# Kernel tuning notes

Measured on AMD Instinct MI355X. Metric: run time of the kernel, lower is better.

Reference implementation:

```python
import jax, jax.numpy as jnp
import numpy as np

B, N, E = 64, 20000, 160000
F_TEXT, HID, OUT = 300, 1024, 1664
NEG_SLOPE = 0.2


def setup_inputs() -> dict:
    key = jax.random.key(0)
    ks = jax.random.split(key, 9)
    img_feat = jax.random.normal(ks[0], (B, OUT), dtype=jnp.float32)
    node_features = jax.random.normal(ks[1], (N, F_TEXT), dtype=jnp.float32)
    edge_src = jax.random.randint(ks[2], (E,), 0, N, dtype=jnp.int32)
    edge_dst = jax.random.randint(ks[3], (E,), 0, N, dtype=jnp.int32)
    edge_weight = jax.random.uniform(ks[4], (E,), dtype=jnp.float32)
    W1 = jax.random.normal(ks[5], (F_TEXT, HID), dtype=jnp.float32) / np.sqrt(F_TEXT)
    b1 = jax.random.normal(ks[6], (HID,), dtype=jnp.float32) * 0.01
    W2 = jax.random.normal(ks[7], (HID, OUT), dtype=jnp.float32) / np.sqrt(HID)
    b2 = jax.random.normal(ks[8], (OUT,), dtype=jnp.float32) * 0.01
    return {"img_feat": img_feat, "node_features": node_features,
            "edge_src": edge_src, "edge_dst": edge_dst, "edge_weight": edge_weight,
            "W1": W1, "b1": b1, "W2": W2, "b2": b2}


def _gcn_norm(edge_src, edge_dst, edge_weight, num_nodes):
    # PyG gcn_norm with add_self_loops=False: symmetric degree normalization
    deg = jax.ops.segment_sum(edge_weight, edge_dst, num_segments=num_nodes)
    dinv = jnp.where(deg > 0, jax.lax.rsqrt(deg), 0.0)
    return dinv[edge_src] * edge_weight * dinv[edge_dst]


def _gcn_conv(x, edge_src, edge_dst, norm, W, b):
    # GCNConv: linear transform, then normalized gather -> scatter-add, then bias
    h = x @ W  # [N, out]
    msgs = h[edge_src] * norm[:, None]  # [E, out] gather + scale
    agg = jax.ops.segment_sum(msgs, edge_dst, num_segments=x.shape[0])
    return agg + b


def reference(img_feat, node_features, edge_src, edge_dst, edge_weight, W1, b1, W2, b2):
    num_nodes = node_features.shape[0]
    norm = _gcn_norm(edge_src, edge_dst, edge_weight, num_nodes)
    x = _gcn_conv(node_features, edge_src, edge_dst, norm, W1, b1)
    x = jnp.where(x >= 0, x, NEG_SLOPE * x)  # leaky_relu(0.2)
    x = _gcn_conv(x, edge_src, edge_dst, norm, W2, b2)
    return img_feat @ x.T  # [B, N]
```

## Files before the change

kernel.cpp:

```cpp
#include <hip/hip_runtime.h>
#include <hip/hip_bf16.h>

#define NNODES 20000
#define NEDGES 160000
#define BQ     64
#define FTEXT  300
#define KPAD1  320
#define HIDDIM 1024
#define OUTDIM 1664
#define EB     (NEDGES / 256)
#define SPLITK 13
#define KLEN   (OUTDIM / SPLITK)

typedef __attribute__((ext_vector_type(8))) short short8;
typedef __attribute__((ext_vector_type(4))) float floatx4;

__device__ inline unsigned short f2bf(float f) {
    union { float f; unsigned int u; } v; v.f = f;
    unsigned int r = v.u + 0x7FFF + ((v.u >> 16) & 1);
    return (unsigned short)(r >> 16);
}
__device__ inline float bf2f(unsigned short h) {
    union { unsigned int u; float f; } v; v.u = ((unsigned int)h) << 16;
    return v.f;
}

__device__ inline void gload16(const unsigned short* g, unsigned short* l) {
    __builtin_amdgcn_global_load_lds(
        (const __attribute__((address_space(1))) unsigned int*)g,
        (__attribute__((address_space(3))) unsigned int*)l, 16, 0, 0);
}

#define W1N  (HIDDIM * KPAD1)
#define N1F4 (HIDDIM * OUTDIM / 4)
#define N2F4 (BQ * OUTDIM / 4)
#define N3F4 (NNODES * FTEXT / 4)
__global__ __launch_bounds__(256) void prep_kernel(
        const int* __restrict__ dst, const float* __restrict__ w,
        float* __restrict__ deg, int* __restrict__ cnt,
        const float* __restrict__ W1, unsigned short* __restrict__ W1ch,
        const float* __restrict__ W2, unsigned short* __restrict__ W2b,
        const float* __restrict__ img, unsigned short* __restrict__ imgb,
        const float* __restrict__ nf, unsigned short* __restrict__ nfb) {
    if (blockIdx.x < EB) {
        int e = blockIdx.x * 256 + threadIdx.x;
        int d = dst[e];
        atomicAdd(&deg[d], w[e]);
        atomicAdd(&cnt[d], 1);
        return;
    }
    int i = (blockIdx.x - EB) * 256 + threadIdx.x;
    if (i < W1N) {
        int p   = i / 20480;
        int ww  = i - p * 20480;
        int s   = ww >> 11;
        int lq  = (ww >> 9) & 3;
        int col = (ww >> 3) & 63;
        int j   = ww & 7;
        int n = p * 64 + col;
        int k = s * 32 + lq * 8 + j;
        float v = (k < FTEXT) ? W1[(long)k * HIDDIM + n] : 0.f;
        W1ch[i] = f2bf(v);
        return;
    }
    i -= W1N;
    const float* in; unsigned short* outp; int j;
    if (i < N1F4)                    { in = W2;  outp = W2b;  j = i; }
    else if (i < N1F4 + N2F4)        { in = img; outp = imgb; j = i - N1F4; }
    else if (i < N1F4 + N2F4 + N3F4) { in = nf;  outp = nfb;  j = i - N1F4 - N2F4; }
    else return;
    float4 v = ((const float4*)in)[j];
    ushort4 o;
    o.x = f2bf(v.x); o.y = f2bf(v.y); o.z = f2bf(v.z); o.w = f2bf(v.w);
    ((ushort4*)outp)[j] = o;
}

__global__ __launch_bounds__(1024) void scan_kernel(const int* __restrict__ cnt,
                                                    int* __restrict__ row_start, int N) {
    __shared__ int partial[1024];
    const int CH = 20;
    int t = threadIdx.x;
    int begin = t * CH;
    int nloc = N - begin; if (nloc > CH) nloc = CH; if (nloc < 0) nloc = 0;
    int vals[CH];
    int s = 0;
    if (nloc == CH) {
        #pragma unroll
        for (int i = 0; i < CH / 4; i++) {
            int4 v = ((const int4*)(cnt + begin))[i];
            vals[i*4+0] = v.x; vals[i*4+1] = v.y; vals[i*4+2] = v.z; vals[i*4+3] = v.w;
            s += v.x + v.y + v.z + v.w;
        }
    } else {
        for (int i = 0; i < nloc; i++) { vals[i] = cnt[begin + i]; s += vals[i]; }
    }
    partial[t] = s;
    __syncthreads();
    for (int off = 1; off < 1024; off <<= 1) {
        int v = (t >= off) ? partial[t - off] : 0;
        __syncthreads();
        partial[t] += v;
        __syncthreads();
    }
    int run = (t == 0) ? 0 : partial[t - 1];
    for (int i = 0; i < nloc; i++) { row_start[begin + i] = run; run += vals[i]; }
    if (t == 1023) row_start[N] = partial[1023];
}

__global__ __launch_bounds__(256) void fillgemm_kernel(
        const int* __restrict__ dst, const int* __restrict__ src,
        const float* __restrict__ w, const float* __restrict__ deg,
        const int* __restrict__ row_start, int* __restrict__ cursor,
        int* __restrict__ src_s, float* __restrict__ wnrm_s,
        const unsigned short* __restrict__ imgb, const unsigned short* __restrict__ W2b,
        float* __restrict__ Ztf13) {
    __shared__ unsigned short As[128][40];
    __shared__ unsigned short Bs[64][40];
    if (blockIdx.x < EB) {
        int e = blockIdx.x * 256 + threadIdx.x;
        int d = dst[e], s = src[e];
        float dd = deg[d], ds = deg[s];
        float nv = (ds > 0.f ? rsqrtf(ds) : 0.f) * w[e] * (dd > 0.f ? rsqrtf(dd) : 0.f);
        int pos = row_start[d] + atomicAdd(&cursor[d], 1);
        src_s[pos] = s;
        wnrm_s[pos] = nv;
        return;
    }
    int bb = blockIdx.x - EB;
    int n0 = (bb & 15) * 64;
    int z  = bb >> 4;
    int kbeg = z * KLEN;
    int t = threadIdx.x;
    int wave = t >> 6, lane = t & 63;
    int lm = lane & 15, lq = lane >> 4;
    floatx4 acc[2][4] = {};
    for (int k0 = kbeg; k0 < kbeg + KLEN; k0 += 32) {
        #pragma unroll
        for (int p2 = 0; p2 < 2; p2++) {
            int idx = p2 * 256 + t;
            int r = idx >> 2, c8 = (idx & 3) * 8;
            uint4 v = make_uint4(0, 0, 0, 0);
            if (r < BQ) v = *(const uint4*)(imgb + (long)r * OUTDIM + k0 + c8);
            *(uint4*)&As[r][c8] = v;
        }
        {
            int r = t >> 2, c8 = (t & 3) * 8;
            uint4 v = *(const uint4*)(W2b + (long)(n0 + r) * OUTDIM + k0 + c8);
            *(uint4*)&Bs[r][c8] = v;
        }
        __syncthreads();
        short8 a[2], b[4];
        #pragma unroll
        for (int rt = 0; rt < 2; rt++)
            a[rt] = *(const short8*)&As[wave * 32 + rt * 16 + lm][lq * 8];
        #pragma unroll
        for (int ct = 0; ct < 4; ct++)
            b[ct] = *(const short8*)&Bs[ct * 16 + lm][lq * 8];
        #pragma unroll
        for (int rt = 0; rt < 2; rt++)
            #pragma unroll
            for (int ct = 0; ct < 4; ct++)
                acc[rt][ct] = __builtin_amdgcn_mfma_f32_16x16x32_bf16(
                    a[rt], b[ct], acc[rt][ct], 0, 0, 0);
        __syncthreads();
    }
    #pragma unroll
    for (int rt = 0; rt < 2; rt++)
        #pragma unroll
        for (int r = 0; r < 4; r++) {
            int gm = wave * 32 + rt * 16 + lq * 4 + r;
            if (gm >= BQ) continue;
            #pragma unroll
            for (int ct = 0; ct < 4; ct++)
                Ztf13[(long)z * BQ * HIDDIM + (long)gm * HIDDIM + n0 + ct * 16 + lm]
                    = acc[rt][ct][r];
        }
}

__global__ __launch_bounds__(256) void aggzt_kernel(
        const unsigned short* __restrict__ nfb, const int* __restrict__ row_start,
        const int* __restrict__ src_s, const float* __restrict__ wnrm_s,
        unsigned short* __restrict__ out,
        const float* __restrict__ Ztf13, unsigned short* __restrict__ Zt,
        const float* __restrict__ img, const float* __restrict__ b2,
        float* __restrict__ cvec) {
    __shared__ float red[256];
    if (blockIdx.x < NNODES / 4) {
        int wave = threadIdx.x >> 6, lane = threadIdx.x & 63;
        int d = blockIdx.x * 4 + wave;
        int s0 = row_start[d], s1 = row_start[d + 1];
        float4 acc  = make_float4(0.f, 0.f, 0.f, 0.f);
        float4 acc2 = make_float4(0.f, 0.f, 0.f, 0.f);
        for (int base = s0; base < s1; base += 64) {
            int m = s1 - base; if (m > 64) m = 64;
            int   src_l = (lane < m) ? src_s[base + lane]  : 0;
            float w_l   = (lane < m) ? wnrm_s[base + lane] : 0.f;
            int sj = __shfl(src_l, 0);
            float wj = __shfl(w_l, 0);
            const ushort4* row = (const ushort4*)(nfb + (long)sj * FTEXT);
            ushort4 hv  = row[lane];
            ushort4 hv2 = make_ushort4(0, 0, 0, 0);
            if (lane < 11) hv2 = row[64 + lane];
            for (int j = 0; j < m; j++) {
                ushort4 nv  = make_ushort4(0, 0, 0, 0);
                ushort4 nv2 = make_ushort4(0, 0, 0, 0);
                float wn = 0.f;
                if (j + 1 < m) {
                    int sn = __shfl(src_l, j + 1);
                    wn = __shfl(w_l, j + 1);
                    const ushort4* nrow = (const ushort4*)(nfb + (long)sn * FTEXT);
                    nv = nrow[lane];
                    if (lane < 11) nv2 = nrow[64 + lane];
                }
                acc.x  += bf2f(hv.x)  * wj; acc.y  += bf2f(hv.y)  * wj;
                acc.z  += bf2f(hv.z)  * wj; acc.w  += bf2f(hv.w)  * wj;
                acc2.x += bf2f(hv2.x) * wj; acc2.y += bf2f(hv2.y) * wj;
                acc2.z += bf2f(hv2.z) * wj; acc2.w += bf2f(hv2.w) * wj;
                hv = nv; hv2 = nv2; wj = wn;
            }
        }
        unsigned short* orow = out + (long)d * KPAD1;
        ushort4 o;
        o.x = f2bf(acc.x); o.y = f2bf(acc.y); o.z = f2bf(acc.z); o.w = f2bf(acc.w);
        ((ushort4*)orow)[lane] = o;
        if (lane < 16) {
            ushort4 o2 = make_ushort4(0, 0, 0, 0);
            if (lane < 11) {
                o2.x = f2bf(acc2.x); o2.y = f2bf(acc2.y);
                o2.z = f2bf(acc2.z); o2.w = f2bf(acc2.w);
            }
            ((ushort4*)orow)[64 + lane] = o2;
        }
        return;
    }
    int bb = blockIdx.x - NNODES / 4;
    if (bb < (BQ * HIDDIM) / 256) {
        int i = bb * 256 + threadIdx.x;
        float s = 0.f;
        #pragma unroll
        for (int z = 0; z < SPLITK; z++) s += Ztf13[(long)z * BQ * HIDDIM + i];
        Zt[i] = f2bf(s);
    } else {
        int b = bb - (BQ * HIDDIM) / 256;
        int l = threadIdx.x;
        float v = 0.f;
        for (int f = l; f < OUTDIM; f += 256) v += img[(long)b * OUTDIM + f] * b2[f];
        red[l] = v;
        __syncthreads();
        if (l < 64) {
            v = red[l] + red[l + 64] + red[l + 128] + red[l + 192];
            for (int off = 32; off > 0; off >>= 1) v += __shfl_down(v, off);
            if (l == 0) cvec[b] = v;
        }
    }
}

__global__ __launch_bounds__(256, 3) void xy_gemm(
        const unsigned short* __restrict__ aggNF, const unsigned short* __restrict__ W1ch,
        const float* __restrict__ b1, const unsigned short* __restrict__ Zt,
        float* __restrict__ Y, int M) {
    __shared__ unsigned short Bsh[20480];
    __shared__ unsigned short xs[32][76];
    int t = threadIdx.x;
    int wn = t >> 6, lane = t & 63;
    int lm = lane & 15, lq = lane >> 4;
    int m0 = blockIdx.x * 32;

    short8 afr[2][10];
    #pragma unroll
    for (int rt = 0; rt < 2; rt++) {
        const unsigned short* ap = aggNF + (long)(m0 + rt * 16 + lm) * KPAD1 + lq * 8;
        #pragma unroll
        for (int kk = 0; kk < 10; kk++)
            afr[rt][kk] = *(const short8*)(ap + kk * 32);
    }
    {
        const unsigned short* src = W1ch + t * 8;
        #pragma unroll
        for (int r = 0; r < 10; r++)
            gload16(src + r * 2048, &Bsh[t * 8 + r * 2048]);
    }
    floatx4 yacc[2] = {};
    for (int p = 0; p < 16; p++) {
        __syncthreads();
        floatx4 acc[2] = {};
        #pragma unroll
        for (int s = 0; s < 10; s++) {
            short8 b = *(const short8*)&Bsh[s * 2048 + lq * 512 + (wn * 16 + lm) * 8];
            acc[0] = __builtin_amdgcn_mfma_f32_16x16x32_bf16(afr[0][s], b, acc[0], 0, 0, 0);
            acc[1] = __builtin_amdgcn_mfma_f32_16x16x32_bf16(afr[1][s], b, acc[1], 0, 0, 0);
        }
        {
            int col = wn * 16 + lm;
            float bv = b1[p * 64 + col];
            #pragma unroll
            for (int rt = 0; rt < 2; rt++)
                #pragma unroll
                for (int r = 0; r < 4; r++) {
                    float v = acc[rt][r] + bv;
                    v = v >= 0.f ? v : 0.2f * v;
                    xs[rt * 16 + lq * 4 + r][col] = f2bf(v);
                }
        }
        __syncthreads();
        if (p + 1 < 16) {
            const unsigned short* src = W1ch + (long)(p + 1) * 20480 + t * 8;
            #pragma unroll
            for (int r = 0; r < 10; r++)
                gload16(src + r * 2048, &Bsh[t * 8 + r * 2048]);
        }
        #pragma unroll
        for (int kk = 0; kk < 2; kk++) {
            short8 b = *(const short8*)(Zt + (long)(wn * 16 + lm) * HIDDIM
                                            + p * 64 + kk * 32 + lq * 8);
            #pragma unroll
            for (int rt = 0; rt < 2; rt++) {
                short8 a = *(const short8*)&xs[rt * 16 + lm][kk * 32 + lq * 8];
                yacc[rt] = __builtin_amdgcn_mfma_f32_16x16x32_bf16(a, b, yacc[rt], 0, 0, 0);
            }
        }
    }
    #pragma unroll
    for (int rt = 0; rt < 2; rt++)
        #pragma unroll
        for (int r = 0; r < 4; r++)
            Y[(long)(m0 + rt * 16 + lq * 4 + r) * 64 + wn * 16 + lm] = yacc[rt][r];
}

__global__ __launch_bounds__(256) void outagg_kernel(const float* __restrict__ Y,
        const int* __restrict__ row_start, const int* __restrict__ src_s,
        const float* __restrict__ wnrm_s, const float* __restrict__ c,
        float* __restrict__ out, int N) {
    __shared__ float tile[4][68];
    int d0 = blockIdx.x * 4;
    int t = threadIdx.x;
    int wave = t >> 6, lane = t & 63;
    int d = d0 + wave;
    int s0 = row_start[d], s1 = row_start[d + 1];
    float acc = 0.f;
    for (int base = s0; base < s1; base += 64) {
        int m = s1 - base; if (m > 64) m = 64;
        int   src_l = (lane < m) ? src_s[base + lane]  : 0;
        float w_l   = (lane < m) ? wnrm_s[base + lane] : 0.f;
        int sj = __shfl(src_l, 0);
        float wj = __shfl(w_l, 0);
        float yv = Y[(long)sj * 64 + lane];
        for (int j = 0; j < m; j++) {
            float yn = 0.f, wn = 0.f;
            if (j + 1 < m) {
                int sn = __shfl(src_l, j + 1);
                wn = __shfl(w_l, j + 1);
                yn = Y[(long)sn * 64 + lane];
            }
            acc += wj * yv;
            yv = yn; wj = wn;
        }
    }
    tile[wave][lane] = acc + c[lane];
    __syncthreads();
    int b = t >> 2, j = t & 3;
    out[(long)b * N + d0 + j] = tile[j][b];
}

extern "C" void kernel_launch(void* const* d_in, const int* in_sizes, int n_in,
                              void* d_out, int out_size, void* d_ws, size_t ws_size,
                              hipStream_t stream) {
    const float* img_feat      = (const float*)d_in[0];
    const float* node_features = (const float*)d_in[1];
    const int*   edge_src      = (const int*)d_in[2];
    const int*   edge_dst      = (const int*)d_in[3];
    const float* edge_weight   = (const float*)d_in[4];
    const float* W1            = (const float*)d_in[5];
    const float* b1            = (const float*)d_in[6];
    const float* W2            = (const float*)d_in[7];
    const float* b2            = (const float*)d_in[8];
    float* out = (float*)d_out;

    const int N = NNODES;

    char* ws = (char*)d_ws;
    size_t off = 0;
    auto alloc = [&](size_t bytes) -> void* {
        void* p = ws + off;
        off = (off + bytes + 255) & ~(size_t)255;
        return p;
    };
    float*          deg       = (float*)alloc((size_t)N * 4);
    int*            cnt       = (int*)alloc((size_t)N * 4);
    int*            cursor    = (int*)alloc((size_t)N * 4);
    size_t zero_bytes = off;
    float*          Ztf13     = (float*)alloc((size_t)SPLITK * BQ * HIDDIM * 4);
    float*          Y         = (float*)alloc((size_t)N * BQ * 4);
    int*            row_start = (int*)alloc((size_t)(N + 1) * 4);
    int*            src_s     = (int*)alloc((size_t)NEDGES * 4);
    float*          wnrm_s    = (float*)alloc((size_t)NEDGES * 4);
    unsigned short* aggNF     = (unsigned short*)alloc((size_t)N * KPAD1 * 2);
    unsigned short* W1ch      = (unsigned short*)alloc((size_t)HIDDIM * KPAD1 * 2);
    unsigned short* W2b       = (unsigned short*)alloc((size_t)HIDDIM * OUTDIM * 2);
    unsigned short* imgb      = (unsigned short*)alloc((size_t)BQ * OUTDIM * 2);
    unsigned short* nfb       = (unsigned short*)alloc((size_t)N * FTEXT * 2);
    unsigned short* Zt        = (unsigned short*)alloc((size_t)BQ * HIDDIM * 2);
    float*          cvec      = (float*)alloc((size_t)BQ * 4);

    hipMemsetAsync(ws, 0, zero_bytes, stream);

    int cvb = (W1N + N1F4 + N2F4 + N3F4 + 255) / 256;
    prep_kernel<<<EB + cvb, 256, 0, stream>>>(
        edge_dst, edge_weight, deg, cnt,
        W1, W1ch, W2, W2b, img_feat, imgb, node_features, nfb);

    scan_kernel<<<1, 1024, 0, stream>>>(cnt, row_start, N);

    fillgemm_kernel<<<EB + 16 * SPLITK, 256, 0, stream>>>(
        edge_dst, edge_src, edge_weight, deg, row_start, cursor, src_s, wnrm_s,
        imgb, W2b, Ztf13);

    aggzt_kernel<<<NNODES / 4 + (BQ * HIDDIM) / 256 + BQ, 256, 0, stream>>>(
        nfb, row_start, src_s, wnrm_s, aggNF, Ztf13, Zt, img_feat, b2, cvec);

    xy_gemm<<<NNODES / 32, 256, 0, stream>>>(aggNF, W1ch, b1, Zt, Y, N);

    outagg_kernel<<<N / 4, 256, 0, stream>>>(Y, row_start, src_s, wnrm_s, cvec, out, N);
}
```

Before: 215.6 us.

## Regroup kernels: run scan alongside split-K GEMM, move bias dot and Zt reduce earlier

The single-block prefix scan now runs as one block of a combined kernel that also launches the split-K img×W2 GEMM, so the serial scan overlaps with GEMM work instead of running alone. The scan shrinks to 256 threads that read the counts twice instead of caching them. The img·b2 bias dot moves into the prep kernel. The Zt split-K reduction moves into the CSR fill kernel, which leaves aggregation as its own kernel. The launch count stays the same, but the scan per thread is longer and serial.

```diff
diff --git a/kernel.cpp b/kernel.cpp
--- a/kernel.cpp
+++ b/kernel.cpp
@@ -41,7 +41,9 @@
         const float* __restrict__ W1, unsigned short* __restrict__ W1ch,
         const float* __restrict__ W2, unsigned short* __restrict__ W2b,
         const float* __restrict__ img, unsigned short* __restrict__ imgb,
-        const float* __restrict__ nf, unsigned short* __restrict__ nfb) {
+        const float* __restrict__ nf, unsigned short* __restrict__ nfb,
+        const float* __restrict__ b2, float* __restrict__ cvec) {
+    __shared__ float red[256];
     if (blockIdx.x < EB) {
         int e = blockIdx.x * 256 + threadIdx.x;
         int d = dst[e];
@@ -49,7 +51,21 @@
         atomicAdd(&cnt[d], 1);
         return;
     }
-    int i = (blockIdx.x - EB) * 256 + threadIdx.x;
+    if (blockIdx.x < EB + BQ) {
+        int b = blockIdx.x - EB;
+        int l = threadIdx.x;
+        float v = 0.f;
+        for (int f = l; f < OUTDIM; f += 256) v += img[(long)b * OUTDIM + f] * b2[f];
+        red[l] = v;
+        __syncthreads();
+        if (l < 64) {
+            v = red[l] + red[l + 64] + red[l + 128] + red[l + 192];
+            for (int off = 32; off > 0; off >>= 1) v += __shfl_down(v, off);
+            if (l == 0) cvec[b] = v;
+        }
+        return;
+    }
+    int i = (blockIdx.x - EB - BQ) * 256 + threadIdx.x;
     if (i < W1N) {
         int p   = i / 20480;
         int ww  = i - p * 20480;
@@ -75,47 +91,94 @@
     ((ushort4*)outp)[j] = o;
 }
 
-__global__ __launch_bounds__(1024) void scan_kernel(const int* __restrict__ cnt,
-                                                    int* __restrict__ row_start, int N) {
-    __shared__ int partial[1024];
-    const int CH = 20;
+__global__ __launch_bounds__(256) void scangemm_kernel(
+        const int* __restrict__ cnt, int* __restrict__ row_start,
+        const unsigned short* __restrict__ imgb, const unsigned short* __restrict__ W2b,
+        float* __restrict__ Ztf13) {
+    __shared__ unsigned short As[128][40];
+    __shared__ unsigned short Bs[64][40];
+    __shared__ int partial[256];
+    if (blockIdx.x == 0) {
+        const int CH2 = 79;
+        int t = threadIdx.x;
+        int begin = t * CH2;
+        int nloc = NNODES - begin; if (nloc > CH2) nloc = CH2; if (nloc < 0) nloc = 0;
+        int s = 0;
+        for (int i = 0; i < nloc; i++) s += cnt[begin + i];
+        partial[t] = s;
+        __syncthreads();
+        for (int off = 1; off < 256; off <<= 1) {
+            int v = (t >= off) ? partial[t - off] : 0;
+            __syncthreads();
+            partial[t] += v;
+            __syncthreads();
+        }
+        int run = (t == 0) ? 0 : partial[t - 1];
+        for (int i = 0; i < nloc; i++) {
+            int c = cnt[begin + i];
+            row_start[begin + i] = run;
+            run += c;
+        }
+        if (t == 255) row_start[NNODES] = partial[255];
+        return;
+    }
+    int bb = blockIdx.x - 1;
+    int n0 = (bb & 15) * 64;
+    int z  = bb >> 4;
+    int kbeg = z * KLEN;
     int t = threadIdx.x;
-    int begin = t * CH;
-    int nloc = N - begin; if (nloc > CH) nloc = CH; if (nloc < 0) nloc = 0;
-    int vals[CH];
-    int s = 0;
-    if (nloc == CH) {
-        #pragma unroll
-        for (int i = 0; i < CH / 4; i++) {
-            int4 v = ((const int4*)(cnt + begin))[i];
-            vals[i*4+0] = v.x; vals[i*4+1] = v.y; vals[i*4+2] = v.z; vals[i*4+3] = v.w;
-            s += v.x + v.y + v.z + v.w;
-        }
-    } else {
-        for (int i = 0; i < nloc; i++) { vals[i] = cnt[begin + i]; s += vals[i]; }
-    }
-    partial[t] = s;
-    __syncthreads();
-    for (int off = 1; off < 1024; off <<= 1) {
-        int v = (t >= off) ? partial[t - off] : 0;
-        __syncthreads();
-        partial[t] += v;
-        __syncthreads();
-    }
-    int run = (t == 0) ? 0 : partial[t - 1];
-    for (int i = 0; i < nloc; i++) { row_start[begin + i] = run; run += vals[i]; }
-    if (t == 1023) row_start[N] = partial[1023];
-}
-
-__global__ __launch_bounds__(256) void fillgemm_kernel(
+    int wave = t >> 6, lane = t & 63;
+    int lm = lane & 15, lq = lane >> 4;
+    floatx4 acc[2][4] = {};
+    for (int k0 = kbeg; k0 < kbeg + KLEN; k0 += 32) {
+        #pragma unroll
+        for (int p2 = 0; p2 < 2; p2++) {
+            int idx = p2 * 256 + t;
+            int r = idx >> 2, c8 = (idx & 3) * 8;
+            uint4 v = make_uint4(0, 0, 0, 0);
+            if (r < BQ) v = *(const uint4*)(imgb + (long)r * OUTDIM + k0 + c8);
+            *(uint4*)&As[r][c8] = v;
+        }
+        {
+            int r = t >> 2, c8 = (t & 3) * 8;
+            uint4 v = *(const uint4*)(W2b + (long)(n0 + r) * OUTDIM + k0 + c8);
+            *(uint4*)&Bs[r][c8] = v;
+        }
+        __syncthreads();
+        short8 a[2], b[4];
+        #pragma unroll
+        for (int rt = 0; rt < 2; rt++)
+            a[rt] = *(const short8*)&As[wave * 32 + rt * 16 + lm][lq * 8];
+        #pragma unroll
+        for (int ct = 0; ct < 4; ct++)
+            b[ct] = *(const short8*)&Bs[ct * 16 + lm][lq * 8];
+        #pragma unroll
+        for (int rt = 0; rt < 2; rt++)
+            #pragma unroll
+            for (int ct = 0; ct < 4; ct++)
+                acc[rt][ct] = __builtin_amdgcn_mfma_f32_16x16x32_bf16(
+                    a[rt], b[ct], acc[rt][ct], 0, 0, 0);
+        __syncthreads();
+    }
+    #pragma unroll
+    for (int rt = 0; rt < 2; rt++)
+        #pragma unroll
+        for (int r = 0; r < 4; r++) {
+            int gm = wave * 32 + rt * 16 + lq * 4 + r;
+            if (gm >= BQ) continue;
+            #pragma unroll
+            for (int ct = 0; ct < 4; ct++)
+                Ztf13[(long)z * BQ * HIDDIM + (long)gm * HIDDIM + n0 + ct * 16 + lm]
+                    = acc[rt][ct][r];
+        }
+}
+
+__global__ __launch_bounds__(256) void fillzt_kernel(
         const int* __restrict__ dst, const int* __restrict__ src,
         const float* __restrict__ w, const float* __restrict__ deg,
         const int* __restrict__ row_start, int* __restrict__ cursor,
         int* __restrict__ src_s, float* __restrict__ wnrm_s,
-        const unsigned short* __restrict__ imgb, const unsigned short* __restrict__ W2b,
-        float* __restrict__ Ztf13) {
-    __shared__ unsigned short As[128][40];
-    __shared__ unsigned short Bs[64][40];
+        const float* __restrict__ Ztf13, unsigned short* __restrict__ Zt) {
     if (blockIdx.x < EB) {
         int e = blockIdx.x * 256 + threadIdx.x;
         int d = dst[e], s = src[e];
@@ -126,132 +189,61 @@
         wnrm_s[pos] = nv;
         return;
     }
-    int bb = blockIdx.x - EB;
-    int n0 = (bb & 15) * 64;
-    int z  = bb >> 4;
-    int kbeg = z * KLEN;
-    int t = threadIdx.x;
-    int wave = t >> 6, lane = t & 63;
-    int lm = lane & 15, lq = lane >> 4;
-    floatx4 acc[2][4] = {};
-    for (int k0 = kbeg; k0 < kbeg + KLEN; k0 += 32) {
-        #pragma unroll
-        for (int p2 = 0; p2 < 2; p2++) {
-            int idx = p2 * 256 + t;
-            int r = idx >> 2, c8 = (idx & 3) * 8;
-            uint4 v = make_uint4(0, 0, 0, 0);
-            if (r < BQ) v = *(const uint4*)(imgb + (long)r * OUTDIM + k0 + c8);
-            *(uint4*)&As[r][c8] = v;
-        }
-        {
-            int r = t >> 2, c8 = (t & 3) * 8;
-            uint4 v = *(const uint4*)(W2b + (long)(n0 + r) * OUTDIM + k0 + c8);
-            *(uint4*)&Bs[r][c8] = v;
-        }
-        __syncthreads();
-        short8 a[2], b[4];
-        #pragma unroll
-        for (int rt = 0; rt < 2; rt++)
-            a[rt] = *(const short8*)&As[wave * 32 + rt * 16 + lm][lq * 8];
-        #pragma unroll
-        for (int ct = 0; ct < 4; ct++)
-            b[ct] = *(const short8*)&Bs[ct * 16 + lm][lq * 8];
-        #pragma unroll
-        for (int rt = 0; rt < 2; rt++)
-            #pragma unroll
-            for (int ct = 0; ct < 4; ct++)
-                acc[rt][ct] = __builtin_amdgcn_mfma_f32_16x16x32_bf16(
-                    a[rt], b[ct], acc[rt][ct], 0, 0, 0);
-        __syncthreads();
-    }
+    int i = (blockIdx.x - EB) * 256 + threadIdx.x;
+    float s = 0.f;
     #pragma unroll
-    for (int rt = 0; rt < 2; rt++)
-        #pragma unroll
-        for (int r = 0; r < 4; r++) {
-            int gm = wave * 32 + rt * 16 + lq * 4 + r;
-            if (gm >= BQ) continue;
-            #pragma unroll
-            for (int ct = 0; ct < 4; ct++)
-                Ztf13[(long)z * BQ * HIDDIM + (long)gm * HIDDIM + n0 + ct * 16 + lm]
-                    = acc[rt][ct][r];
-        }
-}
-
-__global__ __launch_bounds__(256) void aggzt_kernel(
+    for (int z = 0; z < SPLITK; z++) s += Ztf13[(long)z * BQ * HIDDIM + i];
+    Zt[i] = f2bf(s);
+}
+
+__global__ __launch_bounds__(256) void aggnf_kernel(
         const unsigned short* __restrict__ nfb, const int* __restrict__ row_start,
         const int* __restrict__ src_s, const float* __restrict__ wnrm_s,
-        unsigned short* __restrict__ out,
-        const float* __restrict__ Ztf13, unsigned short* __restrict__ Zt,
-        const float* __restrict__ img, const float* __restrict__ b2,
-        float* __restrict__ cvec) {
-    __shared__ float red[256];
-    if (blockIdx.x < NNODES / 4) {
-        int wave = threadIdx.x >> 6, lane = threadIdx.x & 63;
-        int d = blockIdx.x * 4 + wave;
-        int s0 = row_start[d], s1 = row_start[d + 1];
-        float4 acc  = make_float4(0.f, 0.f, 0.f, 0.f);
-        float4 acc2 = make_float4(0.f, 0.f, 0.f, 0.f);
-        for (int base = s0; base < s1; base += 64) {
-            int m = s1 - base; if (m > 64) m = 64;
-            int   src_l = (lane < m) ? src_s[base + lane]  : 0;
-            float w_l   = (lane < m) ? wnrm_s[base + lane] : 0.f;
-            int sj = __shfl(src_l, 0);
-            float wj = __shfl(w_l, 0);
-            const ushort4* row = (const ushort4*)(nfb + (long)sj * FTEXT);
-            ushort4 hv  = row[lane];
-            ushort4 hv2 = make_ushort4(0, 0, 0, 0);
-            if (lane < 11) hv2 = row[64 + lane];
-            for (int j = 0; j < m; j++) {
-                ushort4 nv  = make_ushort4(0, 0, 0, 0);
-                ushort4 nv2 = make_ushort4(0, 0, 0, 0);
-                float wn = 0.f;
-                if (j + 1 < m) {
-                    int sn = __shfl(src_l, j + 1);
-                    wn = __shfl(w_l, j + 1);
-                    const ushort4* nrow = (const ushort4*)(nfb + (long)sn * FTEXT);
-                    nv = nrow[lane];
-                    if (lane < 11) nv2 = nrow[64 + lane];
-                }
-                acc.x  += bf2f(hv.x)  * wj; acc.y  += bf2f(hv.y)  * wj;
-                acc.z  += bf2f(hv.z)  * wj; acc.w  += bf2f(hv.w)  * wj;
-                acc2.x += bf2f(hv2.x) * wj; acc2.y += bf2f(hv2.y) * wj;
-                acc2.z += bf2f(hv2.z) * wj; acc2.w += bf2f(hv2.w) * wj;
-                hv = nv; hv2 = nv2; wj = wn;
+        unsigned short* __restrict__ out) {
+    int wave = threadIdx.x >> 6, lane = threadIdx.x & 63;
+    int d = blockIdx.x * 4 + wave;
+    int s0 = row_start[d], s1 = row_start[d + 1];
+    float4 acc  = make_float4(0.f, 0.f, 0.f, 0.f);
+    float4 acc2 = make_float4(0.f, 0.f, 0.f, 0.f);
+    for (int base = s0; base < s1; base += 64) {
+        int m = s1 - base; if (m > 64) m = 64;
+        int   src_l = (lane < m) ? src_s[base + lane]  : 0;
+        float w_l   = (lane < m) ? wnrm_s[base + lane] : 0.f;
+        int sj = __shfl(src_l, 0);
+        float wj = __shfl(w_l, 0);
+        const ushort4* row = (const ushort4*)(nfb + (long)sj * FTEXT);
+        ushort4 hv  = row[lane];
+        ushort4 hv2 = make_ushort4(0, 0, 0, 0);
+        if (lane < 11) hv2 = row[64 + lane];
+        for (int j = 0; j < m; j++) {
+            ushort4 nv  = make_ushort4(0, 0, 0, 0);
+            ushort4 nv2 = make_ushort4(0, 0, 0, 0);
+            float wn = 0.f;
+            if (j + 1 < m) {
+                int sn = __shfl(src_l, j + 1);
+                wn = __shfl(w_l, j + 1);
+                const ushort4* nrow = (const ushort4*)(nfb + (long)sn * FTEXT);
+                nv = nrow[lane];
+                if (lane < 11) nv2 = nrow[64 + lane];
             }
-        }
-        unsigned short* orow = out + (long)d * KPAD1;
-        ushort4 o;
-        o.x = f2bf(acc.x); o.y = f2bf(acc.y); o.z = f2bf(acc.z); o.w = f2bf(acc.w);
-        ((ushort4*)orow)[lane] = o;
-        if (lane < 16) {
-            ushort4 o2 = make_ushort4(0, 0, 0, 0);
-            if (lane < 11) {
-                o2.x = f2bf(acc2.x); o2.y = f2bf(acc2.y);
-                o2.z = f2bf(acc2.z); o2.w = f2bf(acc2.w);
-            }
-            ((ushort4*)orow)[64 + lane] = o2;
-        }
-        return;
-    }
-    int bb = blockIdx.x - NNODES / 4;
-    if (bb < (BQ * HIDDIM) / 256) {
-        int i = bb * 256 + threadIdx.x;
-        float s = 0.f;
-        #pragma unroll
-        for (int z = 0; z < SPLITK; z++) s += Ztf13[(long)z * BQ * HIDDIM + i];
-        Zt[i] = f2bf(s);
-    } else {
-        int b = bb - (BQ * HIDDIM) / 256;
-        int l = threadIdx.x;
-        float v = 0.f;
-        for (int f = l; f < OUTDIM; f += 256) v += img[(long)b * OUTDIM + f] * b2[f];
-        red[l] = v;
-        __syncthreads();
-        if (l < 64) {
-            v = red[l] + red[l + 64] + red[l + 128] + red[l + 192];
-            for (int off = 32; off > 0; off >>= 1) v += __shfl_down(v, off);
-            if (l == 0) cvec[b] = v;
-        }
+            acc.x  += bf2f(hv.x)  * wj; acc.y  += bf2f(hv.y)  * wj;
+            acc.z  += bf2f(hv.z)  * wj; acc.w  += bf2f(hv.w)  * wj;
+            acc2.x += bf2f(hv2.x) * wj; acc2.y += bf2f(hv2.y) * wj;
+            acc2.z += bf2f(hv2.z) * wj; acc2.w += bf2f(hv2.w) * wj;
+            hv = nv; hv2 = nv2; wj = wn;
+        }
+    }
+    unsigned short* orow = out + (long)d * KPAD1;
+    ushort4 o;
+    o.x = f2bf(acc.x); o.y = f2bf(acc.y); o.z = f2bf(acc.z); o.w = f2bf(acc.w);
+    ((ushort4*)orow)[lane] = o;
+    if (lane < 16) {
+        ushort4 o2 = make_ushort4(0, 0, 0, 0);
+        if (lane < 11) {
+            o2.x = f2bf(acc2.x); o2.y = f2bf(acc2.y);
+            o2.z = f2bf(acc2.z); o2.w = f2bf(acc2.w);
+        }
+        ((ushort4*)orow)[64 + lane] = o2;
     }
 }
 
@@ -405,18 +397,19 @@
     hipMemsetAsync(ws, 0, zero_bytes, stream);
 
     int cvb = (W1N + N1F4 + N2F4 + N3F4 + 255) / 256;
-    prep_kernel<<<EB + cvb, 256, 0, stream>>>(
+    prep_kernel<<<EB + BQ + cvb, 256, 0, stream>>>(
         edge_dst, edge_weight, deg, cnt,
-        W1, W1ch, W2, W2b, img_feat, imgb, node_features, nfb);
-
-    scan_kernel<<<1, 1024, 0, stream>>>(cnt, row_start, N);
-
-    fillgemm_kernel<<<EB + 16 * SPLITK, 256, 0, stream>>>(
+        W1, W1ch, W2, W2b, img_feat, imgb, node_features, nfb, b2, cvec);
+
+    scangemm_kernel<<<1 + 16 * SPLITK, 256, 0, stream>>>(
+        cnt, row_start, imgb, W2b, Ztf13);
+
+    fillzt_kernel<<<EB + (BQ * HIDDIM) / 256, 256, 0, stream>>>(
         edge_dst, edge_src, edge_weight, deg, row_start, cursor, src_s, wnrm_s,
-        imgb, W2b, Ztf13);
-
-    aggzt_kernel<<<NNODES / 4 + (BQ * HIDDIM) / 256 + BQ, 256, 0, stream>>>(
-        nfb, row_start, src_s, wnrm_s, aggNF, Ztf13, Zt, img_feat, b2, cvec);
+        Ztf13, Zt);
+
+    aggnf_kernel<<<NNODES / 4, 256, 0, stream>>>(
+        nfb, row_start, src_s, wnrm_s, aggNF);
 
     xy_gemm<<<NNODES / 32, 256, 0, stream>>>(aggNF, W1ch, b1, Zt, Y, N);
 
```

Result: slower. 232.4 us (+7.8%).

## Double-buffer W1 chunks in xy_gemm with narrower tiles and manual waitcnt

Applied to the files above, without the earlier changes.

Reorganizes the fused xy_gemm kernel to process the hidden dimension in 32-column chunks instead of 64, with W1 chunks double-buffered in LDS and prefetched two iterations ahead using explicit vmcnt waits and raw barriers. Waves are remapped to a 2x2 row/column grid so each holds one A-row tile, bias values are preloaded into registers, and the Zt fragments are software-prefetched one step ahead. Dummy global loads keep the vmcnt accounting uniform in the tail iterations. The aim is to overlap global-to-LDS transfers with MFMA work and to cut LDS use for more occupancy. The cost is twice as many barriers per chunk and fragile hand-tuned waitcnt logic.

```diff
diff --git a/kernel.cpp b/kernel.cpp
--- a/kernel.cpp
+++ b/kernel.cpp
@@ -51,13 +51,13 @@
     }
     int i = (blockIdx.x - EB) * 256 + threadIdx.x;
     if (i < W1N) {
-        int p   = i / 20480;
-        int ww  = i - p * 20480;
-        int s   = ww >> 11;
-        int lq  = (ww >> 9) & 3;
-        int col = (ww >> 3) & 63;
+        int p   = i / 10240;
+        int ww  = i - p * 10240;
+        int s   = ww >> 10;
+        int lq  = (ww >> 8) & 3;
+        int col = (ww >> 3) & 31;
         int j   = ww & 7;
-        int n = p * 64 + col;
+        int n = p * 32 + col;
         int k = s * 32 + lq * 8 + j;
         float v = (k < FTEXT) ? W1[(long)k * HIDDIM + n] : 0.f;
         W1ch[i] = f2bf(v);
@@ -259,72 +259,91 @@
         const unsigned short* __restrict__ aggNF, const unsigned short* __restrict__ W1ch,
         const float* __restrict__ b1, const unsigned short* __restrict__ Zt,
         float* __restrict__ Y, int M) {
-    __shared__ unsigned short Bsh[20480];
-    __shared__ unsigned short xs[32][76];
+    __shared__ unsigned short Bsh[2][10240];
+    __shared__ unsigned short xs[32][40];
+    __shared__ unsigned short dmy[512];
     int t = threadIdx.x;
-    int wn = t >> 6, lane = t & 63;
+    int wave = t >> 6, lane = t & 63;
+    int wr = wave >> 1, wc = wave & 1;
     int lm = lane & 15, lq = lane >> 4;
     int m0 = blockIdx.x * 32;
 
-    short8 afr[2][10];
-    #pragma unroll
-    for (int rt = 0; rt < 2; rt++) {
-        const unsigned short* ap = aggNF + (long)(m0 + rt * 16 + lm) * KPAD1 + lq * 8;
+    short8 afr[10];
+    {
+        const unsigned short* ap = aggNF + (long)(m0 + wr * 16 + lm) * KPAD1 + lq * 8;
         #pragma unroll
         for (int kk = 0; kk < 10; kk++)
-            afr[rt][kk] = *(const short8*)(ap + kk * 32);
-    }
+            afr[kk] = *(const short8*)(ap + kk * 32);
+    }
+    float bvs[32];
+    {
+        const float* brow = b1 + wc * 16 + lm;
+        #pragma unroll
+        for (int p = 0; p < 32; p++) bvs[p] = brow[p * 32];
+    }
+    __builtin_amdgcn_sched_barrier(0);
     {
         const unsigned short* src = W1ch + t * 8;
         #pragma unroll
-        for (int r = 0; r < 10; r++)
-            gload16(src + r * 2048, &Bsh[t * 8 + r * 2048]);
+        for (int r = 0; r < 5; r++)
+            gload16(src + r * 2048, &Bsh[0][t * 8 + r * 2048]);
+    }
+    const unsigned short* zrow = Zt + (long)(wave * 16 + lm) * HIDDIM + lq * 8;
+    short8 ztc = *(const short8*)zrow;
+    {
+        const unsigned short* src = W1ch + 10240 + t * 8;
+        #pragma unroll
+        for (int r = 0; r < 5; r++)
+            gload16(src + r * 2048, &Bsh[1][t * 8 + r * 2048]);
     }
     floatx4 yacc[2] = {};
-    for (int p = 0; p < 16; p++) {
-        __syncthreads();
-        floatx4 acc[2] = {};
+    for (int p = 0; p < 32; p++) {
+        asm volatile("s_waitcnt vmcnt(6)" ::: "memory");
+        __builtin_amdgcn_s_barrier();
+        __builtin_amdgcn_sched_barrier(0);
+        floatx4 acc = {};
         #pragma unroll
         for (int s = 0; s < 10; s++) {
-            short8 b = *(const short8*)&Bsh[s * 2048 + lq * 512 + (wn * 16 + lm) * 8];
-            acc[0] = __builtin_amdgcn_mfma_f32_16x16x32_bf16(afr[0][s], b, acc[0], 0, 0, 0);
-            acc[1] = __builtin_amdgcn_mfma_f32_16x16x32_bf16(afr[1][s], b, acc[1], 0, 0, 0);
+            short8 b = *(const short8*)&Bsh[p & 1][s * 1024 + lq * 256
+                                                  + (wc * 16 + lm) * 8];
+            acc = __builtin_amdgcn_mfma_f32_16x16x32_bf16(afr[s], b, acc, 0, 0, 0);
         }
         {
-            int col = wn * 16 + lm;
-            float bv = b1[p * 64 + col];
+            float bv = bvs[p];
             #pragma unroll
-            for (int rt = 0; rt < 2; rt++)
-                #pragma unroll
-                for (int r = 0; r < 4; r++) {
-                    float v = acc[rt][r] + bv;
-                    v = v >= 0.f ? v : 0.2f * v;
-                    xs[rt * 16 + lq * 4 + r][col] = f2bf(v);
-                }
-        }
-        __syncthreads();
-        if (p + 1 < 16) {
-            const unsigned short* src = W1ch + (long)(p + 1) * 20480 + t * 8;
+            for (int r = 0; r < 4; r++) {
+                float v = acc[r] + bv;
+                v = v >= 0.f ? v : 0.2f * v;
+                xs[wr * 16 + lq * 4 + r][wc * 16 + lm] = f2bf(v);
+            }
+        }
+        asm volatile("s_waitcnt lgkmcnt(0)" ::: "memory");
+        __builtin_amdgcn_s_barrier();
+        __builtin_amdgcn_sched_barrier(0);
+        short8 ztn = ztc;
+        if (p + 1 < 32) ztn = *(const short8*)(zrow + (p + 1) * 32);
+        if (p + 2 < 32) {
+            const unsigned short* src = W1ch + (long)(p + 2) * 10240 + t * 8;
             #pragma unroll
-            for (int r = 0; r < 10; r++)
-                gload16(src + r * 2048, &Bsh[t * 8 + r * 2048]);
-        }
-        #pragma unroll
-        for (int kk = 0; kk < 2; kk++) {
-            short8 b = *(const short8*)(Zt + (long)(wn * 16 + lm) * HIDDIM
-                                            + p * 64 + kk * 32 + lq * 8);
+            for (int r = 0; r < 5; r++)
+                gload16(src + r * 2048, &Bsh[p & 1][t * 8 + r * 2048]);
+        } else {
             #pragma unroll
-            for (int rt = 0; rt < 2; rt++) {
-                short8 a = *(const short8*)&xs[rt * 16 + lm][kk * 32 + lq * 8];
-                yacc[rt] = __builtin_amdgcn_mfma_f32_16x16x32_bf16(a, b, yacc[rt], 0, 0, 0);
-            }
-        }
+            for (int r = 0; r < 5; r++)
+                gload16(W1ch + t * 8, &dmy[0]);
+        }
+        #pragma unroll
+        for (int rt = 0; rt < 2; rt++) {
+            short8 a = *(const short8*)&xs[rt * 16 + lm][lq * 8];
+            yacc[rt] = __builtin_amdgcn_mfma_f32_16x16x32_bf16(a, ztc, yacc[rt], 0, 0, 0);
+        }
+        ztc = ztn;
     }
     #pragma unroll
     for (int rt = 0; rt < 2; rt++)
         #pragma unroll
         for (int r = 0; r < 4; r++)
-            Y[(long)(m0 + rt * 16 + lq * 4 + r) * 64 + wn * 16 + lm] = yacc[rt][r];
+            Y[(long)(m0 + rt * 16 + lq * 4 + r) * 64 + wave * 16 + lm] = yacc[rt][r];
 }
 
 __global__ __launch_bounds__(256) void outagg_kernel(const float* __restrict__ Y,
```

Result: no change. 218.7 us (+1.4%).
